# Kernel optimization log

Hardware: AMD Instinct MI355X
Metric: run time of the kernel (lower is better)

## Reference

```python
import jax, jax.numpy as jnp
import numpy as np

N_HEADS = 12
N_GROUPS = 32
EPS = 1e-5


def setup_inputs() -> dict:
    key = jax.random.key(0)
    ks = jax.random.split(key, 6)
    B, C, H, W = 8, 768, 32, 32
    EC, S = 768, 256
    x = jax.random.normal(ks[0], (B, C, H, W), dtype=jnp.float32)
    encoder_out = jax.random.normal(ks[1], (B, EC, S), dtype=jnp.float32)
    gn_w = jnp.ones((C,), jnp.float32)
    gn_b = jnp.zeros((C,), jnp.float32)
    qkv_w = jax.random.normal(ks[2], (3 * C, C), dtype=jnp.float32) * 0.02
    qkv_b = jnp.zeros((3 * C,), jnp.float32)
    enc_w = jax.random.normal(ks[3], (2 * C, EC), dtype=jnp.float32) * 0.02
    enc_b = jnp.zeros((2 * C,), jnp.float32)
    proj_w = jax.random.normal(ks[4], (C, C), dtype=jnp.float32) * 0.02
    proj_b = jnp.zeros((C,), jnp.float32)
    return {"x": x, "encoder_out": encoder_out, "gn_w": gn_w, "gn_b": gn_b,
            "qkv_w": qkv_w, "qkv_b": qkv_b, "enc_w": enc_w, "enc_b": enc_b,
            "proj_w": proj_w, "proj_b": proj_b}


def _group_norm(x, w, b):
    # x: [B, C, T]
    B, C, T = x.shape
    xg = x.reshape(B, N_GROUPS, C // N_GROUPS, T)
    mean = jnp.mean(xg, axis=(2, 3), keepdims=True)
    var = jnp.var(xg, axis=(2, 3), keepdims=True)
    xn = ((xg - mean) * jax.lax.rsqrt(var + EPS)).reshape(B, C, T)
    return xn * w[None, :, None] + b[None, :, None]


def reference(x, encoder_out, gn_w, gn_b, qkv_w, qkv_b, enc_w, enc_b, proj_w, proj_b):
    B, C, Hs, Ws = x.shape
    T = Hs * Ws
    ch = C // N_HEADS
    xf = x.reshape(B, C, T)
    xn = _group_norm(xf, gn_w, gn_b)
    # 1x1 conv == channel matmul
    qkv = jnp.einsum('oc,bct->bot', qkv_w, xn) + qkv_b[None, :, None]  # [B, 3C, T]
    # torch layout: per-head contiguous blocks of [q, k, v]
    qkv = qkv.reshape(B * N_HEADS, 3 * ch, T)
    q, k, v = qkv[:, :ch], qkv[:, ch:2 * ch], qkv[:, 2 * ch:]
    ekv = jnp.einsum('oc,bcs->bos', enc_w, encoder_out) + enc_b[None, :, None]  # [B, 2C, S]
    ekv = ekv.reshape(B * N_HEADS, 2 * ch, -1)
    ek, ev = ekv[:, :ch], ekv[:, ch:]
    k = jnp.concatenate([ek, k], axis=-1)  # [BH, ch, S+T]
    v = jnp.concatenate([ev, v], axis=-1)
    scale = 1.0 / np.sqrt(np.sqrt(ch))
    w = jnp.einsum('bct,bcs->bts', q * scale, k * scale)  # [BH, T, S+T]
    w = jax.nn.softmax(w.astype(jnp.float32), axis=-1).astype(q.dtype)
    a = jnp.einsum('bts,bcs->bct', w, v).reshape(B, C, T)
    h = jnp.einsum('oc,bct->bot', proj_w, a) + proj_b[None, :, None]
    return (xf + h).reshape(B, C, Hs, Ws)
```

## Files before the change

### kernel.cpp

```cpp
#include <hip/hip_runtime.h>

typedef __attribute__((ext_vector_type(8))) short bf16x8;
typedef __attribute__((ext_vector_type(4))) float f32x4;
typedef __attribute__((ext_vector_type(16))) float f32x16;
typedef __attribute__((ext_vector_type(4))) float float4v;
typedef __attribute__((ext_vector_type(4))) unsigned short ushort4v;
typedef __attribute__((ext_vector_type(8))) unsigned short ushort8v;

#define DEVINL __device__ __forceinline__


DEVINL unsigned short f2bf(float f) {
  union { float f; unsigned u; } v; v.f = f;
  unsigned r = (v.u + 0x7fffu + ((v.u >> 16) & 1u)) >> 16;
  return (unsigned short)r;
}
DEVINL unsigned short f2bfr(float f) {
  union { float f; unsigned u; } v; v.f = f;
  return (unsigned short)((v.u + 0x8000u) >> 16);
}
DEVINL float bf2f(unsigned short h) {
  union { unsigned u; float f; } v; v.u = ((unsigned)h) << 16;
  return v.f;
}
DEVINL float exp2a(float x) {
#if __has_builtin(__builtin_amdgcn_exp2f)
  return __builtin_amdgcn_exp2f(x);
#else
  float r; asm("v_exp_f32 %0, %1" : "=v"(r) : "v"(x)); return r;
#endif
}
DEVINL void gload16(const void* g, void* l) {
  __builtin_amdgcn_global_load_lds(
      (const __attribute__((address_space(1))) unsigned*)g,
      (__attribute__((address_space(3))) unsigned*)l, 16, 0, 0);
}
DEVINL void plswap(unsigned& a, unsigned& b) {
  asm("v_permlane32_swap_b32 %0, %1" : "+v"(a), "+v"(b));
}
DEVINL bf16x8 mkfrag(unsigned a, unsigned b, unsigned c, unsigned d) {
  union { unsigned u[4]; bf16x8 v; } x;
  x.u[0] = a; x.u[1] = b; x.u[2] = c; x.u[3] = d;
  return x.v;
}

__global__ __launch_bounds__(256) void k_cvt(const float* __restrict__ s,
                                             unsigned short* __restrict__ d, int n4) {
  int i = blockIdx.x * 256 + threadIdx.x;
  if (i >= n4) return;
  float4v v = *(const float4v*)(s + (size_t)i * 4);
  ushort4v o;
  o[0] = f2bf(v[0]); o[1] = f2bf(v[1]); o[2] = f2bf(v[2]); o[3] = f2bf(v[3]);
  *(ushort4v*)(d + (size_t)i * 4) = o;
}

__global__ __launch_bounds__(256) void k_gn(const float* __restrict__ x,
                                            const float* __restrict__ gw,
                                            const float* __restrict__ gb,
                                            unsigned short* __restrict__ xnt) {
  int g = blockIdx.x, b = blockIdx.y, tid = threadIdx.x;
  const float* xb = x + ((size_t)b * 768 + g * 24) * 1024;
  float s = 0.f, ss = 0.f;
  for (int i = tid; i < 6144; i += 256) {
    float4v v = *(const float4v*)(xb + (size_t)i * 4);
    s += v[0] + v[1] + v[2] + v[3];
    ss += v[0] * v[0] + v[1] * v[1] + v[2] * v[2] + v[3] * v[3];
  }
  #pragma unroll
  for (int o = 32; o > 0; o >>= 1) { s += __shfl_down(s, o); ss += __shfl_down(ss, o); }
  __shared__ float rs[4], rss[4], stat[2];
  int w = tid >> 6;
  if ((tid & 63) == 0) { rs[w] = s; rss[w] = ss; }
  __syncthreads();
  if (tid == 0) {
    float S = rs[0] + rs[1] + rs[2] + rs[3], SS = rss[0] + rss[1] + rss[2] + rss[3];
    float mean = S / 24576.f;
    float var = SS / 24576.f - mean * mean;
    stat[0] = mean; stat[1] = rsqrtf(fmaxf(var, 0.f) + 1e-5f);
  }
  __syncthreads();
  float mean = stat[0], rstd = stat[1];
  float wv[24], bv[24];
  #pragma unroll
  for (int c = 0; c < 24; ++c) { wv[c] = gw[g * 24 + c]; bv[c] = gb[g * 24 + c]; }
  for (int it = 0; it < 4; ++it) {
    int t = it * 256 + tid;
    ushort8v ov[3];
    #pragma unroll
    for (int c = 0; c < 24; ++c) {
      float v = xb[(size_t)c * 1024 + t];
      ov[c >> 3][c & 7] = f2bf((v - mean) * rstd * wv[c] + bv[c]);
    }
    ushort8v* dst = (ushort8v*)(xnt + ((size_t)(b * 1024 + t)) * 768 + g * 24);
    dst[0] = ov[0]; dst[1] = ov[1]; dst[2] = ov[2];
  }
}

__global__ __launch_bounds__(256) void k_enc_tr(const float* __restrict__ enc,
                                                unsigned short* __restrict__ et) {
  int ct = blockIdx.x * 64, st = blockIdx.y * 64, b = blockIdx.z, tid = threadIdx.x;
  __shared__ unsigned short L[64 * 72];
  #pragma unroll
  for (int it = 0; it < 4; ++it) {
    int idx = it * 256 + tid; int r = idx >> 4, ch = idx & 15;
    float4v v = *(const float4v*)(enc + ((size_t)(b * 768 + ct + r)) * 256 + st + ch * 4);
    ushort4v o;
    o[0] = f2bf(v[0]); o[1] = f2bf(v[1]); o[2] = f2bf(v[2]); o[3] = f2bf(v[3]);
    *(ushort4v*)&L[r * 72 + ch * 4] = o;
  }
  __syncthreads();
  #pragma unroll
  for (int it = 0; it < 2; ++it) {
    int idx = it * 256 + tid; int s = idx >> 3, ch = idx & 7;
    ushort8v o;
    #pragma unroll
    for (int j = 0; j < 8; ++j) o[j] = L[(ch * 8 + j) * 72 + s];
    *(ushort8v*)(et + ((size_t)(b * 256 + st + s)) * 768 + ct + ch * 8) = o;
  }
}

__global__ __launch_bounds__(256) void k_vcat(const unsigned short* __restrict__ qkvt,
                                              const unsigned short* __restrict__ ekvt,
                                              unsigned short* __restrict__ vcat) {
  int s0 = blockIdx.x * 64, bh = blockIdx.y, b = bh / 12, h = bh % 12, tid = threadIdx.x;
  __shared__ unsigned short L[64 * 72];
  #pragma unroll
  for (int it = 0; it < 2; ++it) {
    int idx = it * 256 + tid; int s = idx >> 3, ch = idx & 7;
    int sg = s0 + s;
    const unsigned short* src = (sg < 256)
        ? ekvt + ((size_t)(b * 256 + sg)) * 1536 + h * 128 + 64 + ch * 8
        : qkvt + ((size_t)(b * 1024 + sg - 256)) * 2304 + h * 192 + 128 + ch * 8;
    *(ushort8v*)&L[s * 72 + ch * 8] = *(const ushort8v*)src;
  }
  __syncthreads();
  #pragma unroll
  for (int it = 0; it < 2; ++it) {
    int idx = it * 256 + tid; int c = idx >> 3, ch = idx & 7;
    ushort8v o;
    #pragma unroll
    for (int j = 0; j < 8; ++j) o[j] = L[(ch * 8 + j) * 72 + c];
    *(ushort8v*)(vcat + ((size_t)bh * 64 + c) * 1280 + s0 + ch * 8) = o;
  }
}

template <int EPI>
__global__ __launch_bounds__(256) void k_gemm(const unsigned short* __restrict__ A,
                                              const unsigned short* __restrict__ B,
                                              const float* __restrict__ bias,
                                              const float* __restrict__ resid,
                                              void* __restrict__ outp,
                                              int N, int K,
                                              long sA, long sB, long sO, long sR) {
  int bz = blockIdx.z;
  int m0 = blockIdx.x * 128, n0 = blockIdx.y * 128;
  const unsigned short* Ab = A + (size_t)bz * sA + (size_t)m0 * K;
  const unsigned short* Bb = B + (size_t)bz * sB + (size_t)n0 * K;
  __shared__ unsigned short As[128 * 32], Bs[128 * 32];
  int tid = threadIdx.x, lane = tid & 63, w = tid >> 6;
  int ln = lane & 15, lg = lane >> 4;
  int wm = (w >> 1) * 64, wn = (w & 1) * 64;
  int sr = lane >> 2, sc = lane & 3;
  int rA0 = w * 16 + sr, rA1 = w * 16 + 64 + sr;
  const unsigned short* ga0 = Ab + (size_t)rA0 * K + ((sc ^ (rA0 & 3)) * 8);
  const unsigned short* ga1 = Ab + (size_t)rA1 * K + ((sc ^ (rA1 & 3)) * 8);
  const unsigned short* gb0 = Bb + (size_t)rA0 * K + ((sc ^ (rA0 & 3)) * 8);
  const unsigned short* gb1 = Bb + (size_t)rA1 * K + ((sc ^ (rA1 & 3)) * 8);
  unsigned short* la0 = &As[(w * 16) * 32];
  unsigned short* la1 = &As[(w * 16 + 64) * 32];
  unsigned short* lb0 = &Bs[(w * 16) * 32];
  unsigned short* lb1 = &Bs[(w * 16 + 64) * 32];
  int swz = (lg ^ (ln & 3)) * 8;

  f32x4 acc[4][4];
  #pragma unroll
  for (int i = 0; i < 4; ++i)
    #pragma unroll
    for (int j = 0; j < 4; ++j) acc[i][j] = (f32x4){0.f, 0.f, 0.f, 0.f};

  for (int k0 = 0; k0 < K; k0 += 32) {
    gload16(ga0 + k0, la0);
    gload16(ga1 + k0, la1);
    gload16(gb0 + k0, lb0);
    gload16(gb1 + k0, lb1);
    __syncthreads();
    bf16x8 af[4], bfv[4];
    #pragma unroll
    for (int i = 0; i < 4; ++i) af[i] = *(const bf16x8*)&As[(wm + i * 16 + ln) * 32 + swz];
    #pragma unroll
    for (int i = 0; i < 4; ++i) bfv[i] = *(const bf16x8*)&Bs[(wn + i * 16 + ln) * 32 + swz];
    #pragma unroll
    for (int i = 0; i < 4; ++i)
      #pragma unroll
      for (int j = 0; j < 4; ++j)
        acc[i][j] = __builtin_amdgcn_mfma_f32_16x16x32_bf16(af[i], bfv[j], acc[i][j], 0, 0, 0);
    __syncthreads();
  }

  #pragma unroll
  for (int i = 0; i < 4; ++i) {
    #pragma unroll
    for (int j = 0; j < 4; ++j) {
      #pragma unroll
      for (int r = 0; r < 4; ++r) {
        int row = m0 + wm + i * 16 + lg * 4 + r;
        int col = n0 + wn + j * 16 + ln;
        float v = acc[i][j][r];
        if (EPI == 0) {
          v += bias[col];
          ((unsigned short*)outp)[(size_t)bz * sO + (size_t)row * N + col] = f2bf(v);
        } else {
          v += bias[row] + resid[(size_t)bz * sR + (size_t)row * N + col];
          ((float*)outp)[(size_t)bz * sO + (size_t)row * N + col] = v;
        }
      }
    }
  }
}

__global__ __launch_bounds__(256, 3) void k_attn(const unsigned short* __restrict__ qkvt,
                                                 const unsigned short* __restrict__ ekvt,
                                                 const unsigned short* __restrict__ vcat,
                                                 unsigned short* __restrict__ at) {
  int bid = blockIdx.x;
  int swb = (bid & 7) * 96 + (bid >> 3);
  int t0 = (swb & 7) * 128, bh = swb >> 3, b = bh / 12, h = bh % 12;
  int tid = threadIdx.x, w = tid >> 6, lane = tid & 63;
  int ql = lane & 31, hi = lane >> 5;
  __shared__ unsigned short Ks[2][4096], Vs[2][4096];

  const float QSC = 0.125f * 1.44269504089f;
  bf16x8 aq[4];
  const unsigned short* qrow = qkvt + ((size_t)(b * 1024 + t0 + w * 32 + ql)) * 2304 + h * 192;
  #pragma unroll
  for (int jc = 0; jc < 4; ++jc) {
    ushort8v qv = *(const ushort8v*)(qrow + jc * 16 + hi * 8);
    bf16x8 o;
    #pragma unroll
    for (int e = 0; e < 8; ++e) o[e] = (short)f2bf(bf2f(qv[e]) * QSC);
    aq[jc] = o;
  }

  int rloc = w * 16 + (lane >> 3);
  int chunk = (lane & 7) ^ (lane >> 3);
  const unsigned short* ke_st = ekvt + ((size_t)(b * 256 + rloc)) * 1536 + h * 128 + chunk * 8;
  const unsigned short* kq_st = qkvt + ((long)b * 1024 - 256 + rloc) * 2304 + h * 192 + 64 + chunk * 8;
  const unsigned short* v_st  = vcat + ((size_t)(bh * 64 + rloc)) * 1280 + chunk * 8;
  unsigned short* kd = &Ks[0][0] + w * 1024;
  unsigned short* vd = &Vs[0][0] + w * 1024;

  auto stage = [&](int nb, int tn) {
    const unsigned short* ks;
    size_t rstep;
    if (tn < 4) { ks = ke_st + (size_t)tn * 64 * 1536; rstep = 8 * 1536; }
    else        { ks = kq_st + (size_t)tn * 64 * 2304; rstep = 8 * 2304; }
    unsigned short* kdd = kd + nb * 4096;
    unsigned short* vdd = vd + nb * 4096;
    const unsigned short* vs = v_st + tn * 64;
    gload16(ks, kdd);
    gload16(ks + rstep, kdd + 512);
    gload16(vs, vdd);
    gload16(vs + 8 * 1280, vdd + 512);
  };

  stage(0, 0);
  asm volatile("s_waitcnt vmcnt(0)" ::: "memory");
  __syncthreads();

  f32x16 acc0, acc1;
  #pragma unroll
  for (int r = 0; r < 16; ++r) { acc0[r] = 0.f; acc1[r] = 0.f; }
  float m = -1e30f, l = 0.f;
  int xp = (ql & 7) << 4;

  for (int t = 0; t < 20; ++t) {
    int cur = t & 1;
    if (t < 19) stage(cur ^ 1, t + 1);

    f32x16 sf0, sf1;
    #pragma unroll
    for (int r = 0; r < 16; ++r) { sf0[r] = 0.f; sf1[r] = 0.f; }
    const char* kbase = (const char*)&Ks[cur][0] + ql * 128;
    __builtin_amdgcn_s_setprio(1);
    #pragma unroll
    for (int jc = 0; jc < 4; ++jc) {
      int off = (jc * 32 + hi * 16) ^ xp;
      bf16x8 k0f = *(const bf16x8*)(kbase + off);
      bf16x8 k1f = *(const bf16x8*)(kbase + 4096 + off);
      sf0 = __builtin_amdgcn_mfma_f32_32x32x16_bf16(k0f, aq[jc], sf0, 0, 0, 0);
      sf1 = __builtin_amdgcn_mfma_f32_32x32x16_bf16(k1f, aq[jc], sf1, 0, 0, 0);
    }
    __builtin_amdgcn_s_setprio(0);

    float mx[8];
    #pragma unroll
    for (int i = 0; i < 8; ++i)
      mx[i] = fmaxf(fmaxf(sf0[i], sf0[i + 8]), fmaxf(sf1[i], sf1[i + 8]));
    #pragma unroll
    for (int o = 4; o > 0; o >>= 1)
      #pragma unroll
      for (int i = 0; i < 4; ++i)
        if (i < o) mx[i] = fmaxf(mx[i], mx[i + o]);
    float mt = fmaxf(mx[0], __shfl_xor(mx[0], 32));
    if (!__all(mt <= m + 8.f)) {
      float mn = fmaxf(m, mt);
      float al = exp2a(m - mn);
      l *= al;
      #pragma unroll
      for (int r = 0; r < 16; ++r) { acc0[r] *= al; acc1[r] *= al; }
      m = mn;
    }

    const char* vbase = (const char*)&Vs[cur][0] + ql * 128;
    #pragma unroll
    for (int sb = 0; sb < 2; ++sb) {
      unsigned pk[8];
      #pragma unroll
      for (int i = 0; i < 8; ++i) {
        float pa = exp2a((sb ? sf1[2 * i] : sf0[2 * i]) - m);
        float pb = exp2a((sb ? sf1[2 * i + 1] : sf0[2 * i + 1]) - m);
        l += pa + pb;
        pk[i] = (unsigned)f2bfr(pa) | ((unsigned)f2bfr(pb) << 16);
      }
      plswap(pk[0], pk[2]);
      plswap(pk[1], pk[3]);
      plswap(pk[4], pk[6]);
      plswap(pk[5], pk[7]);
      bf16x8 fj0 = mkfrag(pk[0], pk[1], pk[2], pk[3]);
      bf16x8 fj1 = mkfrag(pk[4], pk[5], pk[6], pk[7]);
      __builtin_amdgcn_s_setprio(1);
      #pragma unroll
      for (int jj = 0; jj < 2; ++jj) {
        int off = (sb * 64 + jj * 32 + hi * 16) ^ xp;
        bf16x8 v0f = *(const bf16x8*)(vbase + off);
        bf16x8 v1f = *(const bf16x8*)(vbase + 4096 + off);
        bf16x8 pf = jj ? fj1 : fj0;
        acc0 = __builtin_amdgcn_mfma_f32_32x32x16_bf16(v0f, pf, acc0, 0, 0, 0);
        acc1 = __builtin_amdgcn_mfma_f32_32x32x16_bf16(v1f, pf, acc1, 0, 0, 0);
      }
      __builtin_amdgcn_s_setprio(0);
    }

    if (t < 19) asm volatile("s_waitcnt vmcnt(0)" ::: "memory");
    __syncthreads();
  }

  l += __shfl_xor(l, 32);
  float rl = 1.f / l;
  unsigned short* orow = at + ((size_t)(b * 1024 + t0 + w * 32 + ql)) * 768 + h * 64;
  #pragma unroll
  for (int cb = 0; cb < 2; ++cb) {
    #pragma unroll
    for (int g = 0; g < 4; ++g) {
      int c = cb * 32 + g * 8 + hi * 4;
      ushort4v o;
      #pragma unroll
      for (int i = 0; i < 4; ++i) {
        float v = (cb ? acc1[g * 4 + i] : acc0[g * 4 + i]) * rl;
        o[i] = f2bf(v);
      }
      *(ushort4v*)(orow + c) = o;
    }
  }
}

extern "C" void kernel_launch(void* const* d_in, const int* in_sizes, int n_in,
                              void* d_out, int out_size, void* d_ws, size_t ws_size,
                              hipStream_t stream) {
  const float* x      = (const float*)d_in[0];
  const float* enc    = (const float*)d_in[1];
  const float* gn_w   = (const float*)d_in[2];
  const float* gn_b   = (const float*)d_in[3];
  const float* qkv_w  = (const float*)d_in[4];
  const float* qkv_b  = (const float*)d_in[5];
  const float* enc_w  = (const float*)d_in[6];
  const float* enc_b  = (const float*)d_in[7];
  const float* proj_w = (const float*)d_in[8];
  const float* proj_b = (const float*)d_in[9];
  float* out = (float*)d_out;

  char* ws = (char*)d_ws;
  unsigned short* w_qkv = (unsigned short*)(ws + 0);
  unsigned short* w_enc = (unsigned short*)(ws + 3538944);
  unsigned short* w_prj = (unsigned short*)(ws + 5898240);
  unsigned short* xn_t  = (unsigned short*)(ws + 7077888);
  unsigned short* enc_t = (unsigned short*)(ws + 19660800);
  unsigned short* qkv_t = (unsigned short*)(ws + 22806528);
  unsigned short* ekv_t = (unsigned short*)(ws + 60555264);
  unsigned short* vcat  = (unsigned short*)(ws + 66846720);
  unsigned short* a_t   = xn_t;

  k_cvt<<<1728, 256, 0, stream>>>(qkv_w, w_qkv, 442368);
  k_cvt<<<1152, 256, 0, stream>>>(enc_w, w_enc, 294912);
  k_cvt<<<576, 256, 0, stream>>>(proj_w, w_prj, 147456);
  k_gn<<<dim3(32, 8), 256, 0, stream>>>(x, gn_w, gn_b, xn_t);
  k_enc_tr<<<dim3(12, 4, 8), 256, 0, stream>>>(enc, enc_t);
  k_gemm<0><<<dim3(8, 18, 8), 256, 0, stream>>>(xn_t, w_qkv, qkv_b, nullptr, qkv_t,
                                                2304, 768, 786432L, 0L, 2359296L, 0L);
  k_gemm<0><<<dim3(2, 12, 8), 256, 0, stream>>>(enc_t, w_enc, enc_b, nullptr, ekv_t,
                                                1536, 768, 196608L, 0L, 393216L, 0L);
  k_vcat<<<dim3(20, 96), 256, 0, stream>>>(qkv_t, ekv_t, vcat);
  k_attn<<<dim3(768), 256, 0, stream>>>(qkv_t, ekv_t, vcat, a_t);
  k_gemm<1><<<dim3(6, 8, 8), 256, 0, stream>>>(w_prj, a_t, proj_b, x, out,
                                               1024, 768, 0L, 786432L, 786432L, 786432L);
}
```

Baseline: 192.6 us.

## Double-buffer GEMM with 64-wide K tiles, lazy softmax rescale, fused weight conversion

The GEMM now stages 64-wide K tiles into double-buffered LDS with an XOR swizzle and prefetches the next tile while MFMAs run. It also sets launch bounds for two blocks per CU and flattens the batch dimension into the M grid for the QKV and encoder projections. Attention computes exp against a stale running max, packs probabilities with a hardware bf16 convert, and rescales only when a probability exceeds 256, taking the max reduction off the critical path. The three weight conversions merge into one launch. Double buffering raises LDS use and may limit occupancy, and the deferred max relies on exp values staying within fp32 range.

```diff
diff --git a/kernel.cpp b/kernel.cpp
--- a/kernel.cpp
+++ b/kernel.cpp
@@ -15,20 +15,17 @@
   unsigned r = (v.u + 0x7fffu + ((v.u >> 16) & 1u)) >> 16;
   return (unsigned short)r;
 }
-DEVINL unsigned short f2bfr(float f) {
-  union { float f; unsigned u; } v; v.f = f;
-  return (unsigned short)((v.u + 0x8000u) >> 16);
-}
 DEVINL float bf2f(unsigned short h) {
   union { unsigned u; float f; } v; v.u = ((unsigned)h) << 16;
   return v.f;
 }
 DEVINL float exp2a(float x) {
-#if __has_builtin(__builtin_amdgcn_exp2f)
-  return __builtin_amdgcn_exp2f(x);
-#else
   float r; asm("v_exp_f32 %0, %1" : "=v"(r) : "v"(x)); return r;
-#endif
+}
+DEVINL unsigned cvtpk(float lo, float hi) {
+  unsigned r;
+  asm("v_cvt_pk_bf16_f32 %0, %1, %2" : "=v"(r) : "v"(lo), "v"(hi));
+  return r;
 }
 DEVINL void gload16(const void* g, void* l) {
   __builtin_amdgcn_global_load_lds(
@@ -44,11 +41,16 @@
   return x.v;
 }
 
-__global__ __launch_bounds__(256) void k_cvt(const float* __restrict__ s,
-                                             unsigned short* __restrict__ d, int n4) {
+__global__ __launch_bounds__(256) void k_cvt3(const float* __restrict__ s0,
+                                              const float* __restrict__ s1,
+                                              const float* __restrict__ s2,
+                                              unsigned short* __restrict__ d) {
   int i = blockIdx.x * 256 + threadIdx.x;
-  if (i >= n4) return;
-  float4v v = *(const float4v*)(s + (size_t)i * 4);
+  const float* s; int off;
+  if (i < 442368)      { s = s0; off = i; }
+  else if (i < 737280) { s = s1; off = i - 442368; }
+  else                 { s = s2; off = i - 737280; }
+  float4v v = *(const float4v*)(s + (size_t)off * 4);
   ushort4v o;
   o[0] = f2bf(v[0]); o[1] = f2bf(v[1]); o[2] = f2bf(v[2]); o[3] = f2bf(v[3]);
   *(ushort4v*)(d + (size_t)i * 4) = o;
@@ -145,32 +147,25 @@
 }
 
 template <int EPI>
-__global__ __launch_bounds__(256) void k_gemm(const unsigned short* __restrict__ A,
-                                              const unsigned short* __restrict__ B,
-                                              const float* __restrict__ bias,
-                                              const float* __restrict__ resid,
-                                              void* __restrict__ outp,
-                                              int N, int K,
-                                              long sA, long sB, long sO, long sR) {
+__global__ __launch_bounds__(256, 2) void k_gemm(const unsigned short* __restrict__ A,
+                                                 const unsigned short* __restrict__ B,
+                                                 const float* __restrict__ bias,
+                                                 const float* __restrict__ resid,
+                                                 void* __restrict__ outp,
+                                                 int N, int K,
+                                                 long sA, long sB, long sO, long sR) {
   int bz = blockIdx.z;
   int m0 = blockIdx.x * 128, n0 = blockIdx.y * 128;
   const unsigned short* Ab = A + (size_t)bz * sA + (size_t)m0 * K;
   const unsigned short* Bb = B + (size_t)bz * sB + (size_t)n0 * K;
-  __shared__ unsigned short As[128 * 32], Bs[128 * 32];
+  __shared__ unsigned short As[2][8192], Bs[2][8192];
   int tid = threadIdx.x, lane = tid & 63, w = tid >> 6;
   int ln = lane & 15, lg = lane >> 4;
   int wm = (w >> 1) * 64, wn = (w & 1) * 64;
-  int sr = lane >> 2, sc = lane & 3;
-  int rA0 = w * 16 + sr, rA1 = w * 16 + 64 + sr;
-  const unsigned short* ga0 = Ab + (size_t)rA0 * K + ((sc ^ (rA0 & 3)) * 8);
-  const unsigned short* ga1 = Ab + (size_t)rA1 * K + ((sc ^ (rA1 & 3)) * 8);
-  const unsigned short* gb0 = Bb + (size_t)rA0 * K + ((sc ^ (rA0 & 3)) * 8);
-  const unsigned short* gb1 = Bb + (size_t)rA1 * K + ((sc ^ (rA1 & 3)) * 8);
-  unsigned short* la0 = &As[(w * 16) * 32];
-  unsigned short* la1 = &As[(w * 16 + 64) * 32];
-  unsigned short* lb0 = &Bs[(w * 16) * 32];
-  unsigned short* lb1 = &Bs[(w * 16 + 64) * 32];
-  int swz = (lg ^ (ln & 3)) * 8;
+  int srow = tid >> 3;
+  int schunk = ((tid & 7) ^ (srow & 7)) * 8;
+  const unsigned short* gA = Ab + (size_t)srow * K + schunk;
+  const unsigned short* gB = Bb + (size_t)srow * K + schunk;
 
   f32x4 acc[4][4];
   #pragma unroll
@@ -178,22 +173,41 @@
     #pragma unroll
     for (int j = 0; j < 4; ++j) acc[i][j] = (f32x4){0.f, 0.f, 0.f, 0.f};
 
-  for (int k0 = 0; k0 < K; k0 += 32) {
-    gload16(ga0 + k0, la0);
-    gload16(ga1 + k0, la1);
-    gload16(gb0 + k0, lb0);
-    gload16(gb1 + k0, lb1);
-    __syncthreads();
-    bf16x8 af[4], bfv[4];
-    #pragma unroll
-    for (int i = 0; i < 4; ++i) af[i] = *(const bf16x8*)&As[(wm + i * 16 + ln) * 32 + swz];
-    #pragma unroll
-    for (int i = 0; i < 4; ++i) bfv[i] = *(const bf16x8*)&Bs[(wn + i * 16 + ln) * 32 + swz];
-    #pragma unroll
-    for (int i = 0; i < 4; ++i)
+  auto stageAB = [&](int buf, int k0) {
+    #pragma unroll
+    for (int it = 0; it < 4; ++it)
+      gload16(gA + (size_t)it * 32 * K + k0, &As[buf][it * 2048 + w * 512]);
+    #pragma unroll
+    for (int it = 0; it < 4; ++it)
+      gload16(gB + (size_t)it * 32 * K + k0, &Bs[buf][it * 2048 + w * 512]);
+  };
+
+  stageAB(0, 0);
+  asm volatile("s_waitcnt vmcnt(0)" ::: "memory");
+  __syncthreads();
+
+  int nk = K >> 6;
+  for (int kt = 0; kt < nk; ++kt) {
+    int cur = kt & 1;
+    if (kt + 1 < nk) stageAB(cur ^ 1, (kt + 1) * 64);
+    #pragma unroll
+    for (int kk = 0; kk < 2; ++kk) {
+      bf16x8 af[4], bfv[4];
+      #pragma unroll
+      for (int i = 0; i < 4; ++i)
+        af[i] = *(const bf16x8*)&As[cur][(wm + i * 16 + ln) * 64 + (((kk * 4 + lg) ^ (ln & 7)) * 8)];
       #pragma unroll
       for (int j = 0; j < 4; ++j)
-        acc[i][j] = __builtin_amdgcn_mfma_f32_16x16x32_bf16(af[i], bfv[j], acc[i][j], 0, 0, 0);
+        bfv[j] = *(const bf16x8*)&Bs[cur][(wn + j * 16 + ln) * 64 + (((kk * 4 + lg) ^ (ln & 7)) * 8)];
+      __builtin_amdgcn_s_setprio(1);
+      #pragma unroll
+      for (int i = 0; i < 4; ++i)
+        #pragma unroll
+        for (int j = 0; j < 4; ++j)
+          acc[i][j] = __builtin_amdgcn_mfma_f32_16x16x32_bf16(af[i], bfv[j], acc[i][j], 0, 0, 0);
+      __builtin_amdgcn_s_setprio(0);
+    }
+    if (kt + 1 < nk) asm volatile("s_waitcnt vmcnt(0)" ::: "memory");
     __syncthreads();
   }
 
@@ -270,7 +284,7 @@
   f32x16 acc0, acc1;
   #pragma unroll
   for (int r = 0; r < 16; ++r) { acc0[r] = 0.f; acc1[r] = 0.f; }
-  float m = -1e30f, l = 0.f;
+  float m = 0.f, l = 0.f;
   int xp = (ql & 7) << 4;
 
   for (int t = 0; t < 20; ++t) {
@@ -292,36 +306,19 @@
     }
     __builtin_amdgcn_s_setprio(0);
 
-    float mx[8];
-    #pragma unroll
-    for (int i = 0; i < 8; ++i)
-      mx[i] = fmaxf(fmaxf(sf0[i], sf0[i + 8]), fmaxf(sf1[i], sf1[i + 8]));
-    #pragma unroll
-    for (int o = 4; o > 0; o >>= 1)
-      #pragma unroll
-      for (int i = 0; i < 4; ++i)
-        if (i < o) mx[i] = fmaxf(mx[i], mx[i + o]);
-    float mt = fmaxf(mx[0], __shfl_xor(mx[0], 32));
-    if (!__all(mt <= m + 8.f)) {
-      float mn = fmaxf(m, mt);
-      float al = exp2a(m - mn);
-      l *= al;
-      #pragma unroll
-      for (int r = 0; r < 16; ++r) { acc0[r] *= al; acc1[r] *= al; }
-      m = mn;
-    }
+    float pe[32];
+    #pragma unroll
+    for (int i = 0; i < 16; ++i) pe[i] = exp2a(sf0[i] - m);
+    #pragma unroll
+    for (int i = 0; i < 16; ++i) pe[16 + i] = exp2a(sf1[i] - m);
 
     const char* vbase = (const char*)&Vs[cur][0] + ql * 128;
     #pragma unroll
     for (int sb = 0; sb < 2; ++sb) {
       unsigned pk[8];
       #pragma unroll
-      for (int i = 0; i < 8; ++i) {
-        float pa = exp2a((sb ? sf1[2 * i] : sf0[2 * i]) - m);
-        float pb = exp2a((sb ? sf1[2 * i + 1] : sf0[2 * i + 1]) - m);
-        l += pa + pb;
-        pk[i] = (unsigned)f2bfr(pa) | ((unsigned)f2bfr(pb) << 16);
-      }
+      for (int i = 0; i < 8; ++i)
+        pk[i] = cvtpk(pe[sb * 16 + 2 * i], pe[sb * 16 + 2 * i + 1]);
       plswap(pk[0], pk[2]);
       plswap(pk[1], pk[3]);
       plswap(pk[4], pk[6]);
@@ -339,6 +336,32 @@
         acc1 = __builtin_amdgcn_mfma_f32_32x32x16_bf16(v1f, pf, acc1, 0, 0, 0);
       }
       __builtin_amdgcn_s_setprio(0);
+    }
+
+    float s0 = 0.f, s1 = 0.f, s2 = 0.f, s3 = 0.f;
+    #pragma unroll
+    for (int i = 0; i < 8; ++i) {
+      s0 += pe[i]; s1 += pe[8 + i]; s2 += pe[16 + i]; s3 += pe[24 + i];
+    }
+    l += (s0 + s1) + (s2 + s3);
+
+    float mx[8];
+    #pragma unroll
+    for (int i = 0; i < 8; ++i)
+      mx[i] = fmaxf(fmaxf(pe[i], pe[i + 8]), fmaxf(pe[i + 16], pe[i + 24]));
+    #pragma unroll
+    for (int o = 4; o > 0; o >>= 1)
+      #pragma unroll
+      for (int i = 0; i < 4; ++i)
+        if (i < o) mx[i] = fmaxf(mx[i], mx[i + o]);
+    float pmax = fmaxf(mx[0], __shfl_xor(mx[0], 32));
+    if (!__all(pmax <= 256.f)) {
+      float mn = m + __log2f(fmaxf(pmax, 1.f));
+      float al = exp2a(m - mn);
+      l *= al;
+      #pragma unroll
+      for (int r = 0; r < 16; ++r) { acc0[r] *= al; acc1[r] *= al; }
+      m = mn;
     }
 
     if (t < 19) asm volatile("s_waitcnt vmcnt(0)" ::: "memory");
@@ -390,15 +413,13 @@
   unsigned short* vcat  = (unsigned short*)(ws + 66846720);
   unsigned short* a_t   = xn_t;
 
-  k_cvt<<<1728, 256, 0, stream>>>(qkv_w, w_qkv, 442368);
-  k_cvt<<<1152, 256, 0, stream>>>(enc_w, w_enc, 294912);
-  k_cvt<<<576, 256, 0, stream>>>(proj_w, w_prj, 147456);
+  k_cvt3<<<3456, 256, 0, stream>>>(qkv_w, enc_w, proj_w, w_qkv);
   k_gn<<<dim3(32, 8), 256, 0, stream>>>(x, gn_w, gn_b, xn_t);
   k_enc_tr<<<dim3(12, 4, 8), 256, 0, stream>>>(enc, enc_t);
-  k_gemm<0><<<dim3(8, 18, 8), 256, 0, stream>>>(xn_t, w_qkv, qkv_b, nullptr, qkv_t,
-                                                2304, 768, 786432L, 0L, 2359296L, 0L);
-  k_gemm<0><<<dim3(2, 12, 8), 256, 0, stream>>>(enc_t, w_enc, enc_b, nullptr, ekv_t,
-                                                1536, 768, 196608L, 0L, 393216L, 0L);
+  k_gemm<0><<<dim3(64, 18, 1), 256, 0, stream>>>(xn_t, w_qkv, qkv_b, nullptr, qkv_t,
+                                                 2304, 768, 0L, 0L, 0L, 0L);
+  k_gemm<0><<<dim3(16, 12, 1), 256, 0, stream>>>(enc_t, w_enc, enc_b, nullptr, ekv_t,
+                                                 1536, 768, 0L, 0L, 0L, 0L);
   k_vcat<<<dim3(20, 96), 256, 0, stream>>>(qkv_t, ekv_t, vcat);
   k_attn<<<dim3(768), 256, 0, stream>>>(qkv_t, ekv_t, vcat, a_t);
   k_gemm<1><<<dim3(6, 8, 8), 256, 0, stream>>>(w_prj, a_t, proj_b, x, out,
```

Measured after the change: 173.4 us. 10.0% less time.
